# Performance work log

Hardware: AMD Instinct MI355X
Metric: run time of the kernel (lower is better)

The kernel has to match this reference:

```python
import jax, jax.numpy as jnp
import numpy as np

# config matching init_kwargs
C = 256; G = 16; GC = C // G; K = 3; P = K * K
PAD = 1; STR = 1; DIL = 1; OFFSET_SCALE = 1.0
N, H, W = 8, 64, 64


def setup_inputs() -> dict:
    key = jax.random.key(0)
    ks = jax.random.split(key, 8)
    def rn(k, shape, sc):
        return jax.random.normal(k, shape, jnp.float32) * sc
    return {
        "x": jax.random.normal(ks[0], (N, H, W, C), jnp.float32),
        "dw_w": rn(ks[1], (C, 1, K, K), 0.1),          # depthwise conv weight (OIHW, groups=C)
        "dw_b": jnp.zeros((C,), jnp.float32),
        "ln_g": jnp.ones((C,), jnp.float32),
        "ln_b": jnp.zeros((C,), jnp.float32),
        "off_w": rn(ks[2], (G * P * 2, C), 0.01),      # offset head (small so offsets stay sane)
        "off_b": jnp.zeros((G * P * 2,), jnp.float32),
        "mask_w": rn(ks[3], (G * P, C), 0.01),
        "mask_b": jnp.zeros((G * P,), jnp.float32),
        "in_w": rn(ks[4], (C, C), 0.05),
        "in_b": jnp.zeros((C,), jnp.float32),
        "out_w": rn(ks[5], (C, C), 0.05),
        "out_b": jnp.zeros((C,), jnp.float32),
    }


def _layer_norm(x, g, b, eps=1e-6):
    m = x.mean(-1, keepdims=True)
    v = ((x - m) ** 2).mean(-1, keepdims=True)
    return (x - m) * jax.lax.rsqrt(v + eps) * g + b


def _grid_sample_bilinear(img, grid):
    # img: (B, Cc, Hh, Ww); grid: (B, L, P, 2) normalized to [-1, 1], (x, y) order.
    # Matches torch.grid_sample(mode='bilinear', padding_mode='zeros', align_corners=False).
    B, Cc, Hh, Ww = img.shape
    gx = (grid[..., 0] + 1.0) * (Ww * 0.5) - 0.5
    gy = (grid[..., 1] + 1.0) * (Hh * 0.5) - 0.5
    x0 = jnp.floor(gx); y0 = jnp.floor(gy)
    tx = gx - x0; ty = gy - y0
    img_f = img.reshape(B, Cc, Hh * Ww)
    def corner(xi, yi, w):
        valid = (xi >= 0) & (xi < Ww) & (yi >= 0) & (yi < Hh)
        idx = (jnp.clip(yi, 0, Hh - 1) * Ww + jnp.clip(xi, 0, Ww - 1)).astype(jnp.int32)
        v = jnp.take_along_axis(img_f, idx.reshape(B, 1, -1), axis=2)  # (B, Cc, L*P)
        return v * (w * valid).reshape(B, 1, -1)
    out = (corner(x0, y0, (1 - tx) * (1 - ty)) + corner(x0 + 1, y0, tx * (1 - ty))
           + corner(x0, y0 + 1, (1 - tx) * ty) + corner(x0 + 1, y0 + 1, tx * ty))
    return out.reshape(B, Cc, grid.shape[1], grid.shape[2])  # (B, Cc, L, P)


def _dcnv3_core(x, offset, mask):
    # x: (N,H,W,C) value features; offset: (N,H,W,G*P*2); mask: (N,H,W,G*P)
    xpad = jnp.pad(x, ((0, 0), (PAD, PAD), (PAD, PAD), (0, 0)))
    Hi, Wi = H + 2 * PAD, W + 2 * PAD
    Ho, Wo = H, W
    # reference points (centers of receptive field), normalized by padded size
    start = (DIL * (K - 1)) // 2 + 0.5
    ry = (start + jnp.arange(Ho, dtype=jnp.float32) * STR) / Hi
    rx = (start + jnp.arange(Wo, dtype=jnp.float32) * STR) / Wi
    ref = jnp.stack([jnp.broadcast_to(rx[None, :], (Ho, Wo)),
                     jnp.broadcast_to(ry[:, None], (Ho, Wo))], -1)  # (Ho,Wo,2) (x,y)
    # dilation grid, x-major flattening to match torch meshgrid('ij') ordering
    d = jnp.arange(K, dtype=jnp.float32) * DIL - (DIL * (K - 1)) // 2
    kgrid = jnp.stack([jnp.repeat(d, K) / Wi, jnp.tile(d, K) / Hi], -1)  # (P,2)
    off = offset.reshape(N, Ho, Wo, G, P, 2)
    norm = jnp.array([Wi, Hi], jnp.float32)
    loc = (ref[None, :, :, None, None, :]
           + kgrid[None, None, None, None, :, :] * OFFSET_SCALE
           + off * OFFSET_SCALE / norm)                      # (N,Ho,Wo,G,P,2)
    sg = (2.0 * loc - 1.0).reshape(N, Ho * Wo, G, P, 2)
    sg = sg.transpose(0, 2, 1, 3, 4).reshape(N * G, Ho * Wo, P, 2)
    val = xpad.reshape(N, Hi * Wi, G * GC).transpose(0, 2, 1).reshape(N * G, GC, Hi, Wi)
    samp = _grid_sample_bilinear(val, sg)                    # (N*G, GC, Ho*Wo, P)
    m = mask.reshape(N, Ho * Wo, G, P).transpose(0, 2, 1, 3).reshape(N * G, 1, Ho * Wo, P)
    out = (samp * m).sum(-1)                                 # (N*G, GC, Ho*Wo)
    return out.reshape(N, G * GC, Ho * Wo).transpose(0, 2, 1).reshape(N, Ho, Wo, C)


def reference(x, dw_w, dw_b, ln_g, ln_b, off_w, off_b, mask_w, mask_b, in_w, in_b, out_w, out_b):
    xp = x @ in_w.T + in_b                                   # input_proj (values)
    # depthwise conv -> LN (channels_last) -> exact GELU
    y = jax.lax.conv_general_dilated(
        x.transpose(0, 3, 1, 2), dw_w, (1, 1), ((PAD, PAD), (PAD, PAD)),
        feature_group_count=C, dimension_numbers=('NCHW', 'OIHW', 'NCHW'))
    y = y + dw_b[None, :, None, None]
    x1 = jax.nn.gelu(_layer_norm(y.transpose(0, 2, 3, 1), ln_g, ln_b), approximate=False)
    offset = x1 @ off_w.T + off_b                            # (N,H,W,G*P*2)
    mlogits = (x1 @ mask_w.T + mask_b).reshape(N, H, W, G, P)
    mask = jax.nn.softmax(mlogits, axis=-1).reshape(N, H, W, G * P)
    out = _dcnv3_core(xp, offset, mask)
    return out @ out_w.T + out_b
```

## Files before the change

kernel.cpp:

```cpp
#include <hip/hip_runtime.h>


#define LL 32768
#define CC 256

typedef __bf16 bf16;
typedef __bf16 bf16x4 __attribute__((ext_vector_type(4)));
typedef __bf16 bf16x8 __attribute__((ext_vector_type(8)));
typedef float f32x4v __attribute__((ext_vector_type(4)));
typedef float f32x2 __attribute__((ext_vector_type(2)));

__device__ __forceinline__ void gload16(const bf16* g, const bf16* lds_base) {
    __builtin_amdgcn_global_load_lds(
        (const __attribute__((address_space(1))) void*)g,
        (__attribute__((address_space(3))) void*)lds_base, 16, 0, 0);
}

__global__ __launch_bounds__(256) void k_prep(
    const float* __restrict__ in_w, const float* __restrict__ off_w,
    const float* __restrict__ mask_w, const float* __restrict__ out_w,
    const float* __restrict__ dw_w, const float* __restrict__ off_b,
    const float* __restrict__ mask_b,
    bf16* __restrict__ in_h, bf16* __restrict__ hw_h,
    bf16* __restrict__ out_h,
    float* __restrict__ dwT, float* __restrict__ hbias) {
    int idx = blockIdx.x * 256 + threadIdx.x;
    if (idx < 60416) {
        const float* s; bf16* hi; int i;
        if (idx < 16384)      { s = in_w;   hi = in_h;          i = idx; }
        else if (idx < 34816) { s = off_w;  hi = hw_h;          i = idx - 16384; }
        else if (idx < 44032) { s = mask_w; hi = hw_h + 73728;  i = idx - 34816; }
        else                  { s = out_w;  hi = out_h;         i = idx - 44032; }
        float4 v = *(const float4*)(s + (size_t)i * 4);
        bf16x4 h;
        h[0] = (bf16)v.x; h[1] = (bf16)v.y; h[2] = (bf16)v.z; h[3] = (bf16)v.w;
        *(bf16x4*)(hi + (size_t)i * 4) = h;
    } else if (idx < 62720) {
        int e = idx - 60416;
        int c = e & 255, j = e >> 8;
        dwT[j * 256 + c] = dw_w[c * 9 + j];
    } else if (idx < 63232) {
        int e = idx - 62720;
        hbias[e] = (e < 288) ? off_b[e] : (e < 432 ? mask_b[e - 288] : 0.f);
    } else if (idx < 68352) {
        int e = idx - 63232;
        bf16x4 z = {(bf16)0.f, (bf16)0.f, (bf16)0.f, (bf16)0.f};
        *(bf16x4*)(hw_h + 110592 + (size_t)e * 4) = z;
    }
}

__global__ __launch_bounds__(256) void k_dwln(
    const float* __restrict__ x, const float* __restrict__ dwT,
    const float* __restrict__ dw_b, const float* __restrict__ ln_g,
    const float* __restrict__ ln_b, bf16* __restrict__ x1h,
    bf16* __restrict__ xb) {
    int t = threadIdx.x;
    int q = t >> 6, u = t & 63;
    int l = blockIdx.x * 4 + q;
    int w = l & 63, h = (l >> 6) & 63, n = l >> 12;
    int c0 = u * 4;

    float4 acc = *(const float4*)(dw_b + c0);
    float4 xc = {0.f, 0.f, 0.f, 0.f};
#pragma unroll
    for (int kh = 0; kh < 3; ++kh) {
        int hh = h + kh - 1;
        if (hh < 0 || hh >= 64) continue;
#pragma unroll
        for (int kw = 0; kw < 3; ++kw) {
            int ww = w + kw - 1;
            if (ww < 0 || ww >= 64) continue;
            float4 xv = *(const float4*)(x + (size_t)(((n * 64 + hh) * 64) + ww) * CC + c0);
            if (kh == 1 && kw == 1) xc = xv;
            float4 wv = *(const float4*)(dwT + (kh * 3 + kw) * 256 + c0);
            acc.x += xv.x * wv.x; acc.y += xv.y * wv.y;
            acc.z += xv.z * wv.z; acc.w += xv.w * wv.w;
        }
    }
    bf16x4 xcb;
    xcb[0] = (bf16)xc.x; xcb[1] = (bf16)xc.y;
    xcb[2] = (bf16)xc.z; xcb[3] = (bf16)xc.w;
    *(bf16x4*)(xb + (size_t)l * CC + c0) = xcb;

    float s = acc.x + acc.y + acc.z + acc.w;
    float ss = acc.x * acc.x + acc.y * acc.y + acc.z * acc.z + acc.w * acc.w;
#pragma unroll
    for (int d = 1; d < 64; d <<= 1) {
        s += __shfl_xor(s, d);
        ss += __shfl_xor(ss, d);
    }
    float mean = s * (1.0f / 256.0f);
    float var = ss * (1.0f / 256.0f) - mean * mean;
    float rstd = rsqrtf(var + 1e-6f);
    float4 gv = *(const float4*)(ln_g + c0);
    float4 bv = *(const float4*)(ln_b + c0);
    float xn0 = (acc.x - mean) * rstd * gv.x + bv.x;
    float xn1 = (acc.y - mean) * rstd * gv.y + bv.y;
    float xn2 = (acc.z - mean) * rstd * gv.z + bv.z;
    float xn3 = (acc.w - mean) * rstd * gv.w + bv.w;
    bf16x4 oh;
    oh[0] = (bf16)(0.5f * xn0 * (1.0f + erff(xn0 * 0.70710678118654752f)));
    oh[1] = (bf16)(0.5f * xn1 * (1.0f + erff(xn1 * 0.70710678118654752f)));
    oh[2] = (bf16)(0.5f * xn2 * (1.0f + erff(xn2 * 0.70710678118654752f)));
    oh[3] = (bf16)(0.5f * xn3 * (1.0f + erff(xn3 * 0.70710678118654752f)));
    *(bf16x4*)(x1h + (size_t)l * CC + c0) = oh;
}

__device__ __forceinline__ void gemm_core(
    const bf16* __restrict__ A, const bf16* __restrict__ Wh,
    const float* __restrict__ bias, bf16* __restrict__ Cbf,
    int Nout, int mb, int nb) {
    int t = threadIdx.x, wave = t >> 6, lane = t & 63;
    int wm = wave & 1, wn = wave >> 1;
    int fm = lane & 15, fq = lane >> 4;

    __shared__ bf16 smem[16384];

    const bf16* gbase[4];
    int lofs[4];
#pragma unroll
    for (int j = 0; j < 4; ++j) {
        int seg = wave * 4 + j;
        int arr = seg >> 3;
        int row = (seg & 7) * 16 + (lane >> 2);
        int col = (lane & 3) * 8;
        gbase[j] = (arr == 0) ? (A + (size_t)(mb + row) * CC + col)
                              : (Wh + (size_t)(nb + row) * CC + col);
        lofs[j] = seg * 512;
    }

    f32x4v acc[4][4];
#pragma unroll
    for (int i = 0; i < 4; ++i)
#pragma unroll
        for (int j = 0; j < 4; ++j) acc[i][j] = (f32x4v){0.f, 0.f, 0.f, 0.f};

#pragma unroll
    for (int j = 0; j < 4; ++j) gload16(gbase[j], smem + lofs[j]);

    for (int kt = 0; kt < 8; ++kt) {
        const bf16* buf = smem + (kt & 1) * 8192;
        bf16* nxt = smem + ((kt & 1) ^ 1) * 8192;
        __syncthreads();
        if (kt < 7) {
#pragma unroll
            for (int j = 0; j < 4; ++j)
                gload16(gbase[j] + (kt + 1) * 32, nxt + lofs[j]);
        }
        bf16x8 af[4], bfh[4];
#pragma unroll
        for (int i = 0; i < 4; ++i)
            af[i] = *(const bf16x8*)&buf[(wm * 64 + i * 16 + fm) * 32 + fq * 8];
#pragma unroll
        for (int j = 0; j < 4; ++j)
            bfh[j] = *(const bf16x8*)&buf[4096 + (wn * 64 + j * 16 + fm) * 32 + fq * 8];
#pragma unroll
        for (int i = 0; i < 4; ++i)
#pragma unroll
            for (int j = 0; j < 4; ++j)
                acc[i][j] = __builtin_amdgcn_mfma_f32_16x16x32_bf16(
                    af[i], bfh[j], acc[i][j], 0, 0, 0);
    }

#pragma unroll
    for (int j = 0; j < 4; ++j) {
        int n_g = nb + wn * 64 + j * 16 + fm;
        if (n_g >= Nout) continue;
        float bv = bias[n_g];
#pragma unroll
        for (int i = 0; i < 4; ++i) {
            int m_g = mb + wm * 64 + i * 16 + fq * 4;
#pragma unroll
            for (int rg = 0; rg < 4; ++rg)
                Cbf[(size_t)(m_g + rg) * Nout + n_g] = (bf16)(acc[i][j][rg] + bv);
        }
    }
}

__global__ __launch_bounds__(256) void k_gemm_ih(
    const bf16* __restrict__ xb, const bf16* __restrict__ x1h,
    const bf16* __restrict__ in_h, const bf16* __restrict__ hw_h,
    const float* __restrict__ in_b, const float* __restrict__ hbias,
    bf16* __restrict__ xpb, bf16* __restrict__ headb) {
    int mb = blockIdx.x * 128;
    int y = blockIdx.y;
    if (y < 2)
        gemm_core(xb, in_h, in_b, xpb, 256, mb, y * 128);
    else
        gemm_core(x1h, hw_h, hbias, headb, 432, mb, (y - 2) * 128);
}

__global__ __launch_bounds__(256) void k_gemm_out(
    const bf16* __restrict__ A, const bf16* __restrict__ Wh,
    const float* __restrict__ bias, float* __restrict__ C32) {
    int mb = blockIdx.x * 64, nb = blockIdx.y * 128;
    int t = threadIdx.x, wave = t >> 6, lane = t & 63;
    int wm = wave & 1, wn = wave >> 1;
    int fm = lane & 15, fq = lane >> 4;

    __shared__ bf16 smem[12288];

    const bf16* gbase[3];
    int lofs[3];
#pragma unroll
    for (int j = 0; j < 3; ++j) {
        int seg = wave * 3 + j;
        int r16 = (seg < 4) ? seg : (seg - 4);
        int row = r16 * 16 + (lane >> 2);
        int col = (lane & 3) * 8;
        gbase[j] = (seg < 4) ? (A + (size_t)(mb + row) * CC + col)
                             : (Wh + (size_t)(nb + row) * CC + col);
        lofs[j] = seg * 512;
    }

    f32x4v acc[2][4];
#pragma unroll
    for (int i = 0; i < 2; ++i)
#pragma unroll
        for (int j = 0; j < 4; ++j) acc[i][j] = (f32x4v){0.f, 0.f, 0.f, 0.f};

#pragma unroll
    for (int j = 0; j < 3; ++j) gload16(gbase[j], smem + lofs[j]);

    for (int kt = 0; kt < 8; ++kt) {
        const bf16* buf = smem + (kt & 1) * 6144;
        bf16* nxt = smem + ((kt & 1) ^ 1) * 6144;
        __syncthreads();
        if (kt < 7) {
#pragma unroll
            for (int j = 0; j < 3; ++j)
                gload16(gbase[j] + (kt + 1) * 32, nxt + lofs[j]);
        }
        bf16x8 af[2], bfh[4];
#pragma unroll
        for (int i = 0; i < 2; ++i)
            af[i] = *(const bf16x8*)&buf[(wm * 32 + i * 16 + fm) * 32 + fq * 8];
#pragma unroll
        for (int j = 0; j < 4; ++j)
            bfh[j] = *(const bf16x8*)&buf[2048 + (wn * 64 + j * 16 + fm) * 32 + fq * 8];
#pragma unroll
        for (int i = 0; i < 2; ++i)
#pragma unroll
            for (int j = 0; j < 4; ++j)
                acc[i][j] = __builtin_amdgcn_mfma_f32_16x16x32_bf16(
                    af[i], bfh[j], acc[i][j], 0, 0, 0);
    }

#pragma unroll
    for (int j = 0; j < 4; ++j) {
        int n_g = nb + wn * 64 + j * 16 + fm;
        float bv = bias[n_g];
#pragma unroll
        for (int i = 0; i < 2; ++i) {
            int m_g = mb + wm * 32 + i * 16 + fq * 4;
#pragma unroll
            for (int rg = 0; rg < 4; ++rg)
                C32[(size_t)(m_g + rg) * 256 + n_g] = acc[i][j][rg] + bv;
        }
    }
}

__device__ __forceinline__ void mac8(f32x2 acc[4], bf16x8 v, float wt) {
    union { bf16x8 b; unsigned u[4]; } cu;
    cu.b = v;
    f32x2 wv = {wt, wt};
#pragma unroll
    for (int i = 0; i < 4; ++i) {
        f32x2 a;
        a.x = __uint_as_float(cu.u[i] << 16);
        a.y = __uint_as_float(cu.u[i] & 0xffff0000u);
        acc[i] += a * wv;
    }
}

__global__ __launch_bounds__(256) void k_gather(
    const bf16* __restrict__ xp, const bf16* __restrict__ head,
    bf16* __restrict__ rows) {
    int t = threadIdx.x;
    int q = t >> 5, u = t & 31;
    int l = blockIdx.x * 8 + q;
    int w = l & 63, h = (l >> 6) & 63, n = l >> 12;

    __shared__ float CW[8][576];
    __shared__ int BASE[8][144];

    for (int j = u; j < 432; j += 32) CW[q][j] = (float)head[(size_t)l * 432 + j];
    __syncthreads();

    if (u < 16) {
        int g = u;
        float mx = -1e30f;
#pragma unroll
        for (int p = 0; p < 9; ++p) mx = fmaxf(mx, CW[q][288 + g * 9 + p]);
        float s = 0.f, e[9];
#pragma unroll
        for (int p = 0; p < 9; ++p) { e[p] = expf(CW[q][288 + g * 9 + p] - mx); s += e[p]; }
        float inv = 1.0f / s;
#pragma unroll
        for (int p = 0; p < 9; ++p) CW[q][288 + g * 9 + p] = e[p] * inv;
    }
    __syncthreads();

    float4 cwr[5];
    int baser[5];
#pragma unroll
    for (int k = 0; k < 5; ++k) {
        if (k < 4 || u < 16) {
            int ei = u + 32 * k;
            int g = ei / 9, p = ei - g * 9;
            float ox = CW[q][g * 18 + p * 2 + 0];
            float oy = CW[q][g * 18 + p * 2 + 1];
            float m  = CW[q][288 + ei];
            float ax = (float)(w + (p / 3) - 1) + ox;
            float ay = (float)(h + (p % 3) - 1) + oy;
            float x0f = floorf(ax), y0f = floorf(ay);
            int x0 = (int)x0f, y0 = (int)y0f;
            float tx = ax - x0f, ty = ay - y0f;
            int xb, yb;
            float wxa, wxb, wya, wyb;
            if (x0 < 0)       { xb = 0;  wxa = (x0 == -1) ? tx : 0.f; wxb = 0.f; }
            else if (x0 > 62) { xb = 62; wxa = 0.f; wxb = (x0 == 63) ? (1.f - tx) : 0.f; }
            else              { xb = x0; wxa = 1.f - tx; wxb = tx; }
            if (y0 < 0)       { yb = 0;  wya = (y0 == -1) ? ty : 0.f; wyb = 0.f; }
            else if (y0 > 62) { yb = 62; wya = 0.f; wyb = (y0 == 63) ? (1.f - ty) : 0.f; }
            else              { yb = y0; wya = 1.f - ty; wyb = ty; }
            float4 cw;
            cw.x = m * wxa * wya; cw.y = m * wxb * wya;
            cw.z = m * wxa * wyb; cw.w = m * wxb * wyb;
            cwr[k] = cw;
            baser[k] = (n << 20) + (yb * 64 + xb) * 256;
        }
    }
    __syncthreads();
#pragma unroll
    for (int k = 0; k < 5; ++k) {
        if (k < 4 || u < 16) {
            int ei = u + 32 * k;
            *(float4*)&CW[q][ei * 4] = cwr[k];
            BASE[q][ei] = baser[k];
        }
    }
    __syncthreads();

    int g = u >> 1;
    int c0 = g * 16 + (u & 1) * 8;
    const bf16* xpc = xp + c0;
    f32x2 acc[4];
    acc[0] = (f32x2){0.f, 0.f}; acc[1] = (f32x2){0.f, 0.f};
    acc[2] = (f32x2){0.f, 0.f}; acc[3] = (f32x2){0.f, 0.f};
#pragma unroll
    for (int p = 0; p < 9; ++p) {
        int ei = g * 9 + p;
        float4 cw = *(const float4*)&CW[q][ei * 4];
        int base = BASE[q][ei];
        const bf16* p0 = xpc + base;
        const bf16* p1 = p0 + 16384;
        bf16x8 v00 = *(const bf16x8*)(p0);
        bf16x8 v01 = *(const bf16x8*)(p0 + 256);
        bf16x8 v10 = *(const bf16x8*)(p1);
        bf16x8 v11 = *(const bf16x8*)(p1 + 256);
        mac8(acc, v00, cw.x);
        mac8(acc, v01, cw.y);
        mac8(acc, v10, cw.z);
        mac8(acc, v11, cw.w);
    }
    bf16x8 oh;
    oh[0] = (bf16)acc[0].x; oh[1] = (bf16)acc[0].y;
    oh[2] = (bf16)acc[1].x; oh[3] = (bf16)acc[1].y;
    oh[4] = (bf16)acc[2].x; oh[5] = (bf16)acc[2].y;
    oh[6] = (bf16)acc[3].x; oh[7] = (bf16)acc[3].y;
    *(bf16x8*)(rows + (size_t)l * CC + c0) = oh;
}

__device__ __forceinline__ float dot256f(const float* a, const float* wrow) {
    const float4* w4 = (const float4*)wrow;
    float s = 0.f;
#pragma unroll 16
    for (int i = 0; i < 64; ++i) {
        float4 u = w4[i];
        const float* ap = a + i * 4;
        s += ap[0] * u.x + ap[1] * u.y + ap[2] * u.z + ap[3] * u.w;
    }
    return s;
}

__global__ __launch_bounds__(256) void k_inproj_fb(
    const float* __restrict__ x, const float* __restrict__ in_w,
    const float* __restrict__ in_b, float* __restrict__ xp) {
    int l = blockIdx.x;
    int t = threadIdx.x;
    __shared__ float xa[256];
    xa[t] = x[l * CC + t];
    __syncthreads();
    xp[l * CC + t] = dot256f(xa, in_w + t * CC) + in_b[t];
}

__device__ __forceinline__ float fetch_px_fb(const float* base, int yy, int xx) {
    if (xx < 0 || xx >= 64 || yy < 0 || yy >= 64) return 0.f;
    return base[(yy * 64 + xx) * CC];
}

__global__ __launch_bounds__(256) void k_main_fb(
    const float* __restrict__ x, const float* __restrict__ xp,
    const float* __restrict__ dw_w, const float* __restrict__ dw_b,
    const float* __restrict__ ln_g, const float* __restrict__ ln_b,
    const float* __restrict__ off_w, const float* __restrict__ off_b,
    const float* __restrict__ mask_w, const float* __restrict__ mask_b,
    const float* __restrict__ out_w, const float* __restrict__ out_b,
    float* __restrict__ out) {
    int l = blockIdx.x;
    int t = threadIdx.x;
    int w = l & 63, h = (l >> 6) & 63, n = l >> 12;
    __shared__ float x1[256];
    __shared__ float red[256];
    __shared__ float offs[288];
    __shared__ float ms[144];
    __shared__ float row[256];

    float acc = dw_b[t];
#pragma unroll
    for (int kh = 0; kh < 3; ++kh) {
        int hh = h + kh - 1;
        if (hh < 0 || hh >= 64) continue;
#pragma unroll
        for (int kw = 0; kw < 3; ++kw) {
            int ww = w + kw - 1;
            if (ww < 0 || ww >= 64) continue;
            acc += x[(((n * 64 + hh) * 64) + ww) * CC + t] * dw_w[t * 9 + kh * 3 + kw];
        }
    }
    red[t] = acc;
    __syncthreads();
    for (int s = 128; s > 0; s >>= 1) {
        if (t < s) red[t] += red[t + s];
        __syncthreads();
    }
    float mean = red[0] * (1.0f / 256.0f);
    __syncthreads();
    float d = acc - mean;
    red[t] = d * d;
    __syncthreads();
    for (int s = 128; s > 0; s >>= 1) {
        if (t < s) red[t] += red[t + s];
        __syncthreads();
    }
    float var = red[0] * (1.0f / 256.0f);
    float xn = d * rsqrtf(var + 1e-6f) * ln_g[t] + ln_b[t];
    x1[t] = 0.5f * xn * (1.0f + erff(xn * 0.70710678118654752f));
    __syncthreads();

    offs[t] = dot256f(x1, off_w + t * CC) + off_b[t];
    if (t < 32) {
        int j = 256 + t;
        offs[j] = dot256f(x1, off_w + j * CC) + off_b[j];
    }
    if (t < 144) ms[t] = dot256f(x1, mask_w + t * CC) + mask_b[t];
    __syncthreads();

    if (t < 16) {
        int g = t;
        float mx = -1e30f;
#pragma unroll
        for (int p = 0; p < 9; ++p) mx = fmaxf(mx, ms[g * 9 + p]);
        float s = 0.f, e[9];
#pragma unroll
        for (int p = 0; p < 9; ++p) { e[p] = expf(ms[g * 9 + p] - mx); s += e[p]; }
        float inv = 1.0f / s;
#pragma unroll
        for (int p = 0; p < 9; ++p) ms[g * 9 + p] = e[p] * inv;
    }
    __syncthreads();

    int g = t >> 4;
    const float* base = xp + (size_t)n * 64 * 64 * CC + t;
    float acc2 = 0.f;
#pragma unroll
    for (int p = 0; p < 9; ++p) {
        float ox = offs[g * 18 + p * 2 + 0];
        float oy = offs[g * 18 + p * 2 + 1];
        float ax = (float)(w + (p / 3) - 1) + ox;
        float ay = (float)(h + (p % 3) - 1) + oy;
        float x0f = floorf(ax), y0f = floorf(ay);
        int x0 = (int)x0f, y0 = (int)y0f;
        float tx = ax - x0f, ty = ay - y0f;
        float v00 = fetch_px_fb(base, y0, x0);
        float v01 = fetch_px_fb(base, y0, x0 + 1);
        float v10 = fetch_px_fb(base, y0 + 1, x0);
        float v11 = fetch_px_fb(base, y0 + 1, x0 + 1);
        float bl = (v00 * (1.f - tx) + v01 * tx) * (1.f - ty) +
                   (v10 * (1.f - tx) + v11 * tx) * ty;
        acc2 += ms[g * 9 + p] * bl;
    }
    row[t] = acc2;
    __syncthreads();
    out[l * CC + t] = dot256f(row, out_w + t * CC) + out_b[t];
}

extern "C" void kernel_launch(void* const* d_in, const int* in_sizes, int n_in,
                              void* d_out, int out_size, void* d_ws,
                              size_t ws_size, hipStream_t stream) {
    const float* x      = (const float*)d_in[0];
    const float* dw_w   = (const float*)d_in[1];
    const float* dw_b   = (const float*)d_in[2];
    const float* ln_g   = (const float*)d_in[3];
    const float* ln_b   = (const float*)d_in[4];
    const float* off_w  = (const float*)d_in[5];
    const float* off_b  = (const float*)d_in[6];
    const float* mask_w = (const float*)d_in[7];
    const float* mask_b = (const float*)d_in[8];
    const float* in_w   = (const float*)d_in[9];
    const float* in_b   = (const float*)d_in[10];
    const float* out_w  = (const float*)d_in[11];
    const float* out_b  = (const float*)d_in[12];
    float* out = (float*)d_out;

    const size_t szBF    = (size_t)LL * CC * 2;
    const size_t szHEADB = (size_t)LL * 432 * 2;
    const size_t szWB    = 1048576;
    const size_t need    = 3 * szBF + szHEADB + szWB;

    dim3 blk(256);
    if (ws_size >= need) {
        char* p = (char*)d_ws;
        bf16* x1h = (bf16*)p; p += szBF;
        bf16* xpb = (bf16*)p; p += szBF;
        bf16* xb  = (bf16*)p; p += szBF;
        bf16* headb = (bf16*)p; p += szHEADB;
        bf16* in_h  = (bf16*)p; p += 131072;
        bf16* hw_h  = (bf16*)p; p += 262144;
        bf16* out_h = (bf16*)p; p += 131072;
        float* dwT  = (float*)p; p += 9216;
        float* hbias = (float*)p;
        bf16* rows = x1h;

        k_prep<<<dim3(267), blk, 0, stream>>>(in_w, off_w, mask_w, out_w, dw_w,
                                              off_b, mask_b, in_h, hw_h, out_h,
                                              dwT, hbias);
        k_dwln<<<dim3(LL / 4), blk, 0, stream>>>(x, dwT, dw_b, ln_g, ln_b, x1h, xb);
        k_gemm_ih<<<dim3(256, 6), blk, 0, stream>>>(
            xb, x1h, in_h, hw_h, in_b, hbias, xpb, headb);
        k_gather<<<dim3(LL / 8), blk, 0, stream>>>(xpb, headb, rows);
        k_gemm_out<<<dim3(512, 2), blk, 0, stream>>>(rows, out_h, out_b, out);
    } else {
        float* xp = (float*)d_ws;
        k_inproj_fb<<<dim3(LL), blk, 0, stream>>>(x, in_w, in_b, xp);
        k_main_fb<<<dim3(LL), blk, 0, stream>>>(x, xp, dw_w, dw_b, ln_g, ln_b,
                                                off_w, off_b, mask_w, mask_b,
                                                out_w, out_b, out);
    }
}
```

Before: 206.4 us.

## Triple-buffer GEMM LDS pipeline with manual waitcnt and pad head stride

```diff
diff --git a/kernel.cpp b/kernel.cpp
--- a/kernel.cpp
+++ b/kernel.cpp
@@ -3,6 +3,7 @@
 
 #define LL 32768
 #define CC 256
+#define HSTR 448
 
 typedef __bf16 bf16;
 typedef __bf16 bf16x4 __attribute__((ext_vector_type(4)));
@@ -109,12 +110,12 @@
 __device__ __forceinline__ void gemm_core(
     const bf16* __restrict__ A, const bf16* __restrict__ Wh,
     const float* __restrict__ bias, bf16* __restrict__ Cbf,
-    int Nout, int mb, int nb) {
+    int Nout, int cstride, int mb, int nb) {
     int t = threadIdx.x, wave = t >> 6, lane = t & 63;
     int wm = wave & 1, wn = wave >> 1;
     int fm = lane & 15, fq = lane >> 4;
 
-    __shared__ bf16 smem[16384];
+    __shared__ bf16 smem[24576];
 
     const bf16* gbase[4];
     int lofs[4];
@@ -137,16 +138,22 @@
 
 #pragma unroll
     for (int j = 0; j < 4; ++j) gload16(gbase[j], smem + lofs[j]);
-
+#pragma unroll
+    for (int j = 0; j < 4; ++j) gload16(gbase[j] + 32, smem + 8192 + lofs[j]);
+
+#pragma unroll
     for (int kt = 0; kt < 8; ++kt) {
-        const bf16* buf = smem + (kt & 1) * 8192;
-        bf16* nxt = smem + ((kt & 1) ^ 1) * 8192;
-        __syncthreads();
-        if (kt < 7) {
+        if (kt < 7)
+            asm volatile("s_waitcnt vmcnt(4)\n\ts_barrier" ::: "memory");
+        else
+            asm volatile("s_waitcnt vmcnt(0)\n\ts_barrier" ::: "memory");
+        if (kt < 6) {
 #pragma unroll
             for (int j = 0; j < 4; ++j)
-                gload16(gbase[j] + (kt + 1) * 32, nxt + lofs[j]);
-        }
+                gload16(gbase[j] + (kt + 2) * 32,
+                        smem + ((kt + 2) % 3) * 8192 + lofs[j]);
+        }
+        const bf16* buf = smem + (kt % 3) * 8192;
         bf16x8 af[4], bfh[4];
 #pragma unroll
         for (int i = 0; i < 4; ++i)
@@ -172,7 +179,7 @@
             int m_g = mb + wm * 64 + i * 16 + fq * 4;
 #pragma unroll
             for (int rg = 0; rg < 4; ++rg)
-                Cbf[(size_t)(m_g + rg) * Nout + n_g] = (bf16)(acc[i][j][rg] + bv);
+                Cbf[(size_t)(m_g + rg) * cstride + n_g] = (bf16)(acc[i][j][rg] + bv);
         }
     }
 }
@@ -184,10 +191,13 @@
     bf16* __restrict__ xpb, bf16* __restrict__ headb) {
     int mb = blockIdx.x * 128;
     int y = blockIdx.y;
-    if (y < 2)
-        gemm_core(xb, in_h, in_b, xpb, 256, mb, y * 128);
-    else
-        gemm_core(x1h, hw_h, hbias, headb, 432, mb, (y - 2) * 128);
+    const bf16 *A, *W;
+    const float* bs;
+    bf16* Cb;
+    int Nout, cstride, nb;
+    if (y < 2) { A = xb;  W = in_h; bs = in_b;  Cb = xpb;   Nout = 256; cstride = 256;  nb = y * 128; }
+    else       { A = x1h; W = hw_h; bs = hbias; Cb = headb; Nout = 432; cstride = HSTR; nb = (y - 2) * 128; }
+    gemm_core(A, W, bs, Cb, Nout, cstride, mb, nb);
 }
 
 __global__ __launch_bounds__(256) void k_gemm_out(
@@ -198,7 +208,7 @@
     int wm = wave & 1, wn = wave >> 1;
     int fm = lane & 15, fq = lane >> 4;
 
-    __shared__ bf16 smem[12288];
+    __shared__ bf16 smem[18432];
 
     const bf16* gbase[3];
     int lofs[3];
@@ -221,16 +231,22 @@
 
 #pragma unroll
     for (int j = 0; j < 3; ++j) gload16(gbase[j], smem + lofs[j]);
-
+#pragma unroll
+    for (int j = 0; j < 3; ++j) gload16(gbase[j] + 32, smem + 6144 + lofs[j]);
+
+#pragma unroll
     for (int kt = 0; kt < 8; ++kt) {
-        const bf16* buf = smem + (kt & 1) * 6144;
-        bf16* nxt = smem + ((kt & 1) ^ 1) * 6144;
-        __syncthreads();
-        if (kt < 7) {
+        if (kt < 7)
+            asm volatile("s_waitcnt vmcnt(3)\n\ts_barrier" ::: "memory");
+        else
+            asm volatile("s_waitcnt vmcnt(0)\n\ts_barrier" ::: "memory");
+        if (kt < 6) {
 #pragma unroll
             for (int j = 0; j < 3; ++j)
-                gload16(gbase[j] + (kt + 1) * 32, nxt + lofs[j]);
-        }
+                gload16(gbase[j] + (kt + 2) * 32,
+                        smem + ((kt + 2) % 3) * 6144 + lofs[j]);
+        }
+        const bf16* buf = smem + (kt % 3) * 6144;
         bf16x8 af[2], bfh[4];
 #pragma unroll
         for (int i = 0; i < 2; ++i)
@@ -284,7 +300,7 @@
     __shared__ float CW[8][576];
     __shared__ int BASE[8][144];
 
-    for (int j = u; j < 432; j += 32) CW[q][j] = (float)head[(size_t)l * 432 + j];
+    for (int j = u; j < 432; j += 32) CW[q][j] = (float)head[(size_t)l * HSTR + j];
     __syncthreads();
 
     if (u < 16) {
@@ -515,7 +531,7 @@
     float* out = (float*)d_out;
 
     const size_t szBF    = (size_t)LL * CC * 2;
-    const size_t szHEADB = (size_t)LL * 432 * 2;
+    const size_t szHEADB = (size_t)LL * HSTR * 2;
     const size_t szWB    = 1048576;
     const size_t need    = 3 * szBF + szHEADB + szWB;
 
```

New measurement: 196.8 us. -4.7%, faster.
